# Performance work log

Measured on AMD Instinct MI355X. Metric: run time of the kernel, lower is better.

The kernel has to match this reference:

```python
import jax, jax.numpy as jnp
import numpy as np

D_MODEL, EMB_DIM, MLP_ORDER, SEQ_LEN, BATCH = 768, 3, 16, 8192, 8


def setup_inputs() -> dict:
    key = jax.random.key(0)
    ks = jax.random.split(key, 12)
    L = SEQ_LEN
    # PositionalEmbedding buffers (deterministic, as in __init__)
    t = jnp.linspace(0.0, 1.0, L)[None, :, None]                      # [1, L, 1]
    bands = (EMB_DIM - 1) // 2                                        # = 1
    t_long = jnp.linspace(0.0, L - 1.0, L)[None, :, None]
    w = 2.0 * jnp.pi * t_long / L
    f = jnp.linspace(1e-4, bands - 1.0, bands)[None, None]
    zc = jnp.exp(-1j * f * w)
    z = jnp.concatenate([t, zc.real, zc.imag], axis=-1).astype(jnp.float32)  # [1, L, 3]
    # ExponentialModulation deltas (deterministic)
    max_decay = jnp.log(0.01) / 0.3
    min_decay = jnp.log(0.01) / 1.5
    deltas = jnp.linspace(min_decay, max_decay, D_MODEL)[None, None].astype(jnp.float32)  # [1,1,D]
    s = 0.1
    return {
        "x": jax.random.normal(ks[0], (BATCH, D_MODEL, L), jnp.float32),
        "L": L,
        "z": z,
        "t": t.astype(jnp.float32),
        "deltas": deltas,
        "freq": jnp.ones((1, MLP_ORDER), jnp.float32),
        "W0": jax.random.normal(ks[1], (EMB_DIM, MLP_ORDER), jnp.float32) * s,
        "b0": jax.random.normal(ks[2], (MLP_ORDER,), jnp.float32) * s,
        "W1": jax.random.normal(ks[3], (MLP_ORDER, MLP_ORDER), jnp.float32) * s,
        "b1": jax.random.normal(ks[4], (MLP_ORDER,), jnp.float32) * s,
        "W2": jax.random.normal(ks[5], (MLP_ORDER, MLP_ORDER), jnp.float32) * s,
        "b2": jax.random.normal(ks[6], (MLP_ORDER,), jnp.float32) * s,
        "W3": jax.random.normal(ks[7], (MLP_ORDER, D_MODEL), jnp.float32) * s,
        "b3": jax.random.normal(ks[8], (D_MODEL,), jnp.float32) * s,
        "bias": jax.random.normal(ks[9], (D_MODEL,), jnp.float32),
    }


def reference(x, L, z, t, deltas, freq, W0, b0, W1, b1, W2, b2, W3, b3, bias):
    # filter generation: MLP with shared Sin activation, then exponential modulation
    zl = z[:, :L]
    h = jnp.sin(freq * (zl @ W0 + b0))
    h = jnp.sin(freq * (h @ W1 + b1))
    h = jnp.sin(freq * (h @ W2 + b2))
    h = h @ W3 + b3                               # [1, L, D]
    h = h * jnp.exp(-t[:, :L] * jnp.abs(deltas))  # exponential modulation
    k = h[0].T                                    # [D, L]
    # fftconv: causal long convolution via zero-padded FFT + skip x*bias
    fft_size = 2 * L
    y = jnp.fft.irfft(jnp.fft.rfft(x, n=fft_size) * jnp.fft.rfft(k, n=fft_size), n=fft_size)[..., :L]
    return y + x * bias[:, None]
```

## Files before the change

### kernel.cpp

```cpp
#include <hip/hip_runtime.h>
#include <math.h>


#define LSEQ 8192
#define NCH 768
#define NBATCH 8
#define NT 512

#define OFF_TWB  0
#define OFF_TW16 1024
#define OFF_TL   5124
#define OFF_TWC  6660
#define OFF_H    10240
#define OFF_KF   141312

typedef float cplx __attribute__((ext_vector_type(2)));

__device__ __forceinline__ cplx cmul(cplx a, cplx b){
    return cplx{a.x, a.x} * b + cplx{a.y, a.y} * cplx{-b.y, b.x};
}
__device__ __forceinline__ cplx mni(cplx a){ return cplx{a.y, -a.x}; }

__device__ __forceinline__ void wave_sync(){
    asm volatile("s_waitcnt lgkmcnt(0)" ::: "memory");
}
__device__ __forceinline__ void fence(){
    asm volatile("" ::: "memory");
}

__device__ __forceinline__ int IDX14(int i){ return i ^ (((i>>4) ^ (i>>8)) & 14); }
__device__ __forceinline__ int drev(int k){
    return ((k & 15) << 9) | (((k >> 4) & 15) << 5) | (((k >> 8) & 15) << 1) | (k >> 12);
}

#define C1 0.923879532511286756f
#define S1 0.382683432365089772f
#define R2 0.707106781186547524f

template<bool FULL>
__device__ __forceinline__ void dft16(cplx q[16]) {
    if constexpr (FULL) {
#pragma unroll
        for (int j = 0; j < 8; ++j) { cplx u=q[j], v=q[j+8]; q[j]=u+v; q[j+8]=u-v; }
    }
    q[9]  = cmul(q[9],  cplx{ C1,-S1});
    q[10] = cmul(q[10], cplx{ R2,-R2});
    q[11] = cmul(q[11], cplx{ S1,-C1});
    q[12] = mni(q[12]);
    q[13] = cmul(q[13], cplx{-S1,-C1});
    q[14] = cmul(q[14], cplx{-R2,-R2});
    q[15] = cmul(q[15], cplx{-C1,-S1});
#pragma unroll
    for (int b = 0; b < 16; b += 8) {
#pragma unroll
        for (int j = 0; j < 4; ++j) { cplx u=q[b+j], v=q[b+j+4]; q[b+j]=u+v; q[b+j+4]=u-v; }
        q[b+5] = cmul(q[b+5], cplx{ R2,-R2});
        q[b+6] = mni(q[b+6]);
        q[b+7] = cmul(q[b+7], cplx{-R2,-R2});
    }
#pragma unroll
    for (int b = 0; b < 16; b += 4) {
        cplx u0=q[b], v0=q[b+2], u1=q[b+1], v1=q[b+3];
        q[b]=u0+v0; q[b+2]=u0-v0;
        q[b+1]=u1+v1; q[b+3]=mni(u1-v1);
    }
#pragma unroll
    for (int b = 0; b < 16; b += 2) { cplx u=q[b], v=q[b+1]; q[b]=u+v; q[b+1]=u-v; }
}

template<int PASS>
__device__ __forceinline__ int psb(int t) {
    if constexpr (PASS == 0) {
        return t ^ (((t>>4) ^ (t>>8)) & 14);
    } else if constexpr (PASS == 1) {
        int p = t & 31, hb = t >> 5;
        return ((hb<<9) | p) ^ (((p>>4) ^ (hb<<1)) & 14);
    } else {
        int h = t >> 1;
        return ((h<<5) | (t&1)) ^ (((h<<1) ^ (h>>3)) & 14);
    }
}
template<int PASS>
__device__ __forceinline__ int paddr(int sb, int r) {
    if constexpr (PASS == 0)      return (sb ^ (2*(r&7))) + (r<<9);
    else if constexpr (PASS == 1) return (sb ^ (2*(r&7))) + (r<<5);
    else                          return sb ^ (r<<1);
}

template<int PASS, bool DIT, bool PRUNED>
__device__ __forceinline__ void r16p(cplx* lds, const cplx (*twT)[68],
                                     const cplx (&twA)[15], int t) {
    static constexpr int RV[16] = {0,8,4,12,2,10,6,14,1,9,5,13,3,11,7,15};
    const int sb = psb<PASS>(t);
    int rL = 0;
    if constexpr (PASS == 1) { rL = t & 31; }
    else if constexpr (PASS == 2) { rL = 64 + (t & 1); }
    cplx q[16];
    if constexpr (PRUNED) {
#pragma unroll
        for (int r = 0; r < 8; ++r) { q[r] = lds[paddr<PASS>(sb, r)]; q[r+8] = q[r]; }
    } else {
#pragma unroll
        for (int r = 0; r < 16; ++r) q[r] = lds[paddr<PASS>(sb, r)];
    }
    if constexpr (DIT) {
#pragma unroll
        for (int m = 1; m < 16; ++m) {
            cplx w = (PASS == 0) ? twA[m-1] : twT[m][rL];
            q[m] = cmul(q[m], w);
        }
        dft16<true>(q);
    } else {
        dft16<!PRUNED>(q);
#pragma unroll
        for (int m = 1; m < 16; ++m) {
            cplx w = (PASS == 0) ? twA[m-1] : twT[m][rL];
            q[RV[m]] = cmul(q[RV[m]], w);
        }
    }
#pragma unroll
    for (int m = 0; m < 16; ++m) lds[paddr<PASS>(sb, m)] = q[RV[m]];
}

template<int PASS, bool DIT, bool PRUNED>
__device__ __forceinline__ void r16pp(cplx* l0, cplx* l1, const cplx (*twT)[68],
                                      const cplx (&twA)[15], int t) {
    r16p<PASS, DIT, PRUNED>(l0, twT, twA, t);
    fence();
    r16p<PASS, DIT, PRUNED>(l1, twT, twA, t);
}

__device__ __forceinline__ void load_twT(cplx (*twT)[68], const float* __restrict__ ws, int tid) {
    const cplx* gTWB = (const cplx*)(ws + OFF_TWB);
    const cplx* gTL  = (const cplx*)(ws + OFF_TL);
    const cplx* gTWC = (const cplx*)(ws + OFF_TWC);
    for (int idx = tid; idx < 16*66; idx += NT) {
        int r = idx >> 4, m = idx & 15;
        cplx v;
        if (r < 32)      v = gTWB[(r << 4) + m];
        else if (r < 64) v = gTL[((r - 32) << 4) + m];
        else             v = gTWC[((r - 64) << 4) + m];
        twT[m][r] = v;
    }
}

__device__ __forceinline__ void make_twA(cplx (&twA)[15], const cplx (*twT)[68], int t) {
    const int rL = 32 + (t & 31);
    const int rH = (t >> 5) << 1;
#pragma unroll
    for (int m = 1; m < 16; ++m) twA[m-1] = cmul(twT[m][rL], twT[m][rH]);
}

__device__ __forceinline__ void specpair(cplx V1, cplx V2, float4 kv, cplx W,
                                         cplx& o1, cplx& o2) {
    cplx Eh = V1 + cplx{V2.x, -V2.y};
    cplx Oh = cplx{V1.y + V2.y, V2.x - V1.x};
    cplx S = cplx{kv.x, kv.y};
    float a = W.x*kv.z, b = W.y*kv.w, cc = W.x*kv.w, dd = W.y*kv.z;
    cplx T  = cplx{a - b, cc + dd};
    cplx T2 = cplx{a + b, cc - dd};
    cplx Ep = cmul(Eh, S) + cmul(Oh, T);
    cplx Op = cmul(Eh, T2) + cmul(Oh, S);
    o1 = cplx{Ep.y + Op.x, Ep.x - Op.y};
    o2 = cplx{Op.x - Ep.y, Ep.x + Op.y};
}

__device__ __forceinline__ void spec_rows(float4* l4, int sA, int sB,
                                          float4 kvk, float4 kvj, cplx W, cplx Wj) {
    float4 fA = l4[sA], fB = l4[sB];
    cplx uA = {fA.x, fA.y}, vA = {fA.z, fA.w};
    cplx uB = {fB.x, fB.y}, vB = {fB.z, fB.w};
    cplx Vk = uA + vA, Vk4 = uA - vA;
    cplx Vj = uB + vB, Vj4 = uB - vB;
    cplx r1, r2, r1j, r2j;
    specpair(Vk, Vj4, kvk, W,  r1,  r2);
    specpair(Vj, Vk4, kvj, Wj, r1j, r2j);
    cplx a0 = r1 + r2j, a1 = r1 - r2j;
    cplx b0 = r1j + r2, b1 = r1j - r2;
    l4[sA] = make_float4(a0.x, a0.y, a1.x, a1.y);
    l4[sB] = make_float4(b0.x, b0.y, b1.x, b1.y);
}

__device__ __forceinline__ void spec_dc(float4* l4, float4 kv) {
    float4 f = l4[0];
    cplx u = {f.x, f.y}, v = {f.z, f.w};
    cplx V0 = u + v, VN = u - v;
    float U0 = V0.x + V0.y, UL = V0.x - V0.y;
    float re = U0*kv.x + UL*kv.y;
    float im = U0*kv.x - UL*kv.y;
    cplx s0 = {im, re};
    cplx P = {VN.x*kv.z + VN.y*kv.w, VN.x*kv.w - VN.y*kv.z};
    cplx s1 = {-P.y, P.x};
    cplx a = s0 + s1, b = s0 - s1;
    l4[0] = make_float4(a.x, a.y, b.x, b.y);
}

__device__ __forceinline__ void filt_store(const float4* l4, float4* kf, int k, int jj,
                                           int sA, int sB, cplx W, cplx Wj,
                                           float sc, float eb) {
    float4 fA = l4[sA], fB = l4[sB];
    cplx uA = {fA.x, fA.y}, vA = {fA.z, fA.w};
    cplx uB = {fB.x, fB.y}, vB = {fB.z, fB.w};
    cplx Vk = uA + vA, Vk4 = uA - vA;
    cplx Vj = uB + vB, Vj4 = uB - vB;
    {
        cplx E = {Vk.x + Vj4.x + eb, Vk.y - Vj4.y};
        cplx O = {Vk.y + Vj4.y, Vj4.x - Vk.x};
        cplx D = cmul(W, O);
        kf[k] = make_float4(E.x*sc, E.y*sc, D.x*sc, D.y*sc);
    }
    {
        cplx E = {Vj.x + Vk4.x + eb, Vj.y - Vk4.y};
        cplx O = {Vj.y + Vk4.y, Vk4.x - Vj.x};
        cplx D = cmul(Wj, O);
        kf[jj] = make_float4(E.x*sc, E.y*sc, D.x*sc, D.y*sc);
    }
}
__device__ __forceinline__ void filt_dc(const float4* l4, float4* kf, float bc) {
    float4 f = l4[0];
    cplx u = {f.x, f.y}, v = {f.z, f.w};
    cplx V0 = u + v, VN = u - v;
    kf[0] = make_float4((V0.x + V0.y + bc)/16384.f, (V0.x - V0.y + bc)/16384.f,
                        (VN.x + bc)/8192.f, -VN.y/8192.f);
}

__global__ __launch_bounds__(512) void k_pre(const float* __restrict__ z, const float* __restrict__ freq,
        const float* __restrict__ W0, const float* __restrict__ b0,
        const float* __restrict__ W1, const float* __restrict__ b1,
        const float* __restrict__ W2, const float* __restrict__ b2,
        float* __restrict__ ws, float* __restrict__ H) {
    __shared__ double2 lA[128], lB[128];
    const int t = threadIdx.x;
    if (blockIdx.x == 0) {
        const double K = -2.0 * 3.14159265358979323846 / 16384.0;
        if (t < 128)      { double a = K * (double)(t << 7); lA[t] = make_double2(cos(a), sin(a)); }
        else if (t < 256) { int b = t - 128; double a = K * (double)b; lB[b] = make_double2(cos(a), sin(a)); }
        __syncthreads();
        auto wf = [&](int e) -> float2 {
            e &= 16383;
            double2 A = lA[e >> 7], B = lB[e & 127];
            return make_float2((float)(A.x*B.x - A.y*B.y), (float)(A.x*B.y + A.y*B.x));
        };
        float2* tw16 = (float2*)(ws + OFF_TW16);
        for (int k = t; k <= 2048; k += 512) tw16[k] = wf(k);
        if (t < 32) {
            float2* rowL = (float2*)(ws + OFF_TL)  + (t << 4);
            float2* rowB = (float2*)(ws + OFF_TWB) + (t << 4);
#pragma unroll
            for (int m = 0; m < 16; ++m) { rowL[m] = wf(2*t*m); rowB[m] = wf(32*t*m); }
        } else if (t < 34) {
            int c2 = t - 32;
            float2* rowC = (float2*)(ws + OFF_TWC) + (c2 << 4);
#pragma unroll
            for (int m = 0; m < 16; ++m) rowC[m] = wf(512*c2*m);
        }
    } else {
        const int j = ((blockIdx.x - 1) << 9) + t;
        const float z0 = z[j*3+0], z1 = z[j*3+1], z2 = z[j*3+2];
        float h[16], g[16];
#pragma unroll
        for (int m = 0; m < 16; ++m)
            h[m] = sinf(freq[m] * (z0*W0[m] + z1*W0[16+m] + z2*W0[32+m] + b0[m]));
#pragma unroll
        for (int m = 0; m < 16; ++m) {
            float a = b1[m];
#pragma unroll
            for (int p = 0; p < 16; ++p) a += h[p] * W1[p*16+m];
            g[m] = sinf(freq[m] * a);
        }
#pragma unroll
        for (int m = 0; m < 16; ++m) {
            float a = b2[m];
#pragma unroll
            for (int p = 0; p < 16; ++p) a += g[p] * W2[p*16+m];
            h[m] = sinf(freq[m] * a);
        }
        float4* hp = (float4*)(H + (j << 4));
        hp[0] = make_float4(h[0],  h[1],  h[2],  h[3]);
        hp[1] = make_float4(h[4],  h[5],  h[6],  h[7]);
        hp[2] = make_float4(h[8],  h[9],  h[10], h[11]);
        hp[3] = make_float4(h[12], h[13], h[14], h[15]);
    }
}

__global__ __launch_bounds__(NT) void k_filter(const float* __restrict__ H, const float* __restrict__ t,
        const float* __restrict__ deltas, const float* __restrict__ W3,
        const float* __restrict__ b3, const float* __restrict__ bias,
        const float* __restrict__ ws, float* __restrict__ KfF) {
    __shared__ alignas(16) cplx lds2[2][LSEQ];
    __shared__ cplx twT[16][68];
    const int c0 = blockIdx.x << 1, c1 = c0 + 1;
    const int tid = threadIdx.x;
    cplx* l0 = lds2[0];
    cplx* l1 = lds2[1];
    float4* l04 = (float4*)l0;
    float4* l14 = (float4*)l1;
    load_twT(twT, ws, tid);
    float w30[16], w31[16];
#pragma unroll
    for (int m = 0; m < 16; ++m) { w30[m] = W3[m*NCH + c0]; w31[m] = W3[m*NCH + c1]; }
    const float b30 = b3[c0], b31 = b3[c1];
    const float ad0 = fabsf(deltas[c0]), ad1 = fabsf(deltas[c1]);
    const float bc0 = bias[c0], bc1 = bias[c1];
    const int sbA = psb<0>(tid);
#pragma unroll 1
    for (int j = 0; j < 8; ++j) {
        int n = tid + (j << 9);
        const float4* hp = (const float4*)(H + (n << 5));
        float sA0 = b30, sB0 = b30, sA1 = b31, sB1 = b31;
#pragma unroll
        for (int q = 0; q < 4; ++q) {
            float4 a = hp[q];
            float4 b = hp[4+q];
            sA0 += a.x*w30[4*q] + a.y*w30[4*q+1] + a.z*w30[4*q+2] + a.w*w30[4*q+3];
            sB0 += b.x*w30[4*q] + b.y*w30[4*q+1] + b.z*w30[4*q+2] + b.w*w30[4*q+3];
            sA1 += a.x*w31[4*q] + a.y*w31[4*q+1] + a.z*w31[4*q+2] + a.w*w31[4*q+3];
            sB1 += b.x*w31[4*q] + b.y*w31[4*q+1] + b.z*w31[4*q+2] + b.w*w31[4*q+3];
        }
        float2 tv = ((const float2*)t)[n];
        int a0 = paddr<0>(sbA, j);
        float e0 = expf(-tv.x*ad0), e1 = expf(-tv.y*ad0);
        float e2 = expf(-tv.x*ad1), e3 = expf(-tv.y*ad1);
        l0[a0] = cplx{sA0 * e0, sB0 * e1};
        l1[a0] = cplx{sA1 * e2, sB1 * e3};
    }
    __syncthreads();
    cplx twA[15];
    make_twA(twA, twT, tid);
    r16pp<0,false,true >(l0, l1, twT, twA, tid); __syncthreads();
    r16pp<1,false,false>(l0, l1, twT, twA, tid); wave_sync();
    r16pp<2,false,false>(l0, l1, twT, twA, tid); __syncthreads();

    float4* kf0 = (float4*)KfF + (size_t)c0 * 4096;
    float4* kf1 = (float4*)KfF + (size_t)c1 * 4096;
    const cplx* tw16 = (const cplx*)(ws + OFF_TW16);
    const float sc = 1.0f / 32768.0f;
#pragma unroll 1
    for (int it = 0; it < 4; ++it) {
        int k  = tid + 1 + (it << 9);
        int jj = 4096 - k;
        int sA = IDX14(drev(k)) >> 1, sB = IDX14(drev(jj)) >> 1;
        cplx W  = tw16[k];
        cplx Wj = cplx{-W.y, -W.x};
        filt_store(l04, kf0, k, jj, sA, sB, W, Wj, sc, 2.0f*bc0);
        filt_store(l14, kf1, k, jj, sA, sB, W, Wj, sc, 2.0f*bc1);
    }
    if (tid == 0) { filt_dc(l04, kf0, bc0); filt_dc(l14, kf1, bc1); }
}

__global__ __launch_bounds__(NT) void k_main(const float* __restrict__ x, const float* __restrict__ ws,
        const float* __restrict__ KfF, float* __restrict__ out) {
    __shared__ alignas(16) cplx lds2[2][LSEQ];
    __shared__ cplx twT[16][68];
    const int bid = blockIdx.x;
    const int c = bid >> 1, half = bid & 1;
    const int tt = threadIdx.x;
    cplx* l0 = lds2[0];
    cplx* l1 = lds2[1];
    float4* l04 = (float4*)l0;
    float4* l14 = (float4*)l1;
    const float4* kf4 = (const float4*)KfF + (size_t)c * 4096;
    const cplx* tw16 = (const cplx*)(ws + OFF_TW16);
    const size_t rowstride = (size_t)NCH * LSEQ;
    const float* xbase = x + (size_t)(half*4) * rowstride + (size_t)c * LSEQ;
    float* obase = out + (size_t)(half*4) * rowstride + (size_t)c * LSEQ;

    const int EB = (tt << 1) ^ (((tt>>3) ^ (tt>>7)) & 14);

    load_twT(twT, ws, tt);
    __syncthreads();
    cplx twA[15];
    make_twA(twA, twT, tt);

#pragma unroll 1
    for (int pp = 0; pp < 2; ++pp) {
        const float4* xr0 = (const float4*)(xbase + (size_t)(2*pp)     * rowstride);
        const float4* xr1 = (const float4*)(xbase + (size_t)(2*pp + 1) * rowstride);
#pragma unroll
        for (int j = 0; j < 4; ++j) {
            int si = ((EB ^ (j<<2)) + (j<<10)) >> 1;
            l04[si] = xr0[tt + (j<<9)];
            l14[si] = xr1[tt + (j<<9)];
        }
        __syncthreads();
        r16pp<0,false,true >(l0, l1, twT, twA, tt); __syncthreads();
        r16pp<1,false,false>(l0, l1, twT, twA, tt); wave_sync();
        r16pp<2,false,false>(l0, l1, twT, twA, tt); __syncthreads();

#pragma unroll 1
        for (int it = 0; it < 4; ++it) {
            int k  = tt + 1 + (it << 9);
            int jj = 4096 - k;
            int sA = IDX14(drev(k)) >> 1, sB = IDX14(drev(jj)) >> 1;
            float4 kvk = kf4[k], kvj = kf4[jj];
            cplx W  = tw16[k];
            cplx Wj = cplx{-W.y, -W.x};
            spec_rows(l04, sA, sB, kvk, kvj, W, Wj);
            spec_rows(l14, sA, sB, kvk, kvj, W, Wj);
        }
        if (tt == 0) {
            float4 kv = kf4[0];
            spec_dc(l04, kv);
            spec_dc(l14, kv);
        }
        __syncthreads();

        r16pp<2,true,false>(l0, l1, twT, twA, tt); wave_sync();
        r16pp<1,true,false>(l0, l1, twT, twA, tt); __syncthreads();
        r16pp<0,true,false>(l0, l1, twT, twA, tt); __syncthreads();

        float4* o0 = (float4*)(obase + (size_t)(2*pp)     * rowstride);
        float4* o1 = (float4*)(obase + (size_t)(2*pp + 1) * rowstride);
#pragma unroll
        for (int j = 0; j < 4; ++j) {
            int si = ((EB ^ (j<<2)) + (j<<10)) >> 1;
            float4 f0 = l04[si], f1 = l14[si];
            o0[tt + (j<<9)] = make_float4(f0.y, f0.x, f0.w, f0.z);
            o1[tt + (j<<9)] = make_float4(f1.y, f1.x, f1.w, f1.z);
        }
        if (pp == 0) __syncthreads();
    }
}

extern "C" void kernel_launch(void* const* d_in, const int* in_sizes, int n_in,
                              void* d_out, int out_size, void* d_ws, size_t ws_size,
                              hipStream_t stream) {
    const float* x      = (const float*)d_in[0];
    const float* z      = (const float*)d_in[2];
    const float* t      = (const float*)d_in[3];
    const float* deltas = (const float*)d_in[4];
    const float* freq   = (const float*)d_in[5];
    const float* W0     = (const float*)d_in[6];
    const float* b0     = (const float*)d_in[7];
    const float* W1     = (const float*)d_in[8];
    const float* b1     = (const float*)d_in[9];
    const float* W2     = (const float*)d_in[10];
    const float* b2     = (const float*)d_in[11];
    const float* W3     = (const float*)d_in[12];
    const float* b3     = (const float*)d_in[13];
    const float* bias   = (const float*)d_in[14];
    float* out = (float*)d_out;
    float* ws  = (float*)d_ws;
    float* H   = ws + OFF_H;
    float* Kf  = ws + OFF_KF;

    hipLaunchKernelGGL(k_pre, dim3(17), dim3(512), 0, stream, z, freq, W0, b0, W1, b1, W2, b2, ws, H);
    hipLaunchKernelGGL(k_filter, dim3(NCH/2), dim3(NT), 0, stream, H, t, deltas, W3, b3, bias, ws, Kf);
    hipLaunchKernelGGL(k_main, dim3(NBATCH * NCH / 4), dim3(NT), 0, stream, x, ws, Kf, out);
}
```

Measured before the change: 595.6 us.

## Fuse filter spectrum generation into main convolution kernel, one channel per block

Removes the separate k_filter launch. Each k_main block now owns one channel: it builds that channel's modulated MLP filter, runs its forward FFT with the single-sequence r16p path and writes the spectrum to the workspace. It then loops over all 8 batch rows in 4 pairs, reusing the spectrum, instead of 2 blocks per channel doing 2 pairs each. This saves a kernel launch and the inter-kernel dependency. In exchange the grid shrinks to 768 blocks with longer per-block work, and the filter FFT runs unpaired at lower lane efficiency.

After: 574.9 us, median of 2. 1.04x faster.

```diff
diff --git a/kernel.cpp b/kernel.cpp
--- a/kernel.cpp
+++ b/kernel.cpp
@@ -283,99 +283,84 @@
     }
 }
 
-__global__ __launch_bounds__(NT) void k_filter(const float* __restrict__ H, const float* __restrict__ t,
-        const float* __restrict__ deltas, const float* __restrict__ W3,
-        const float* __restrict__ b3, const float* __restrict__ bias,
-        const float* __restrict__ ws, float* __restrict__ KfF) {
+__global__ __launch_bounds__(NT) void k_main(const float* __restrict__ x, const float* __restrict__ H,
+        const float* __restrict__ t, const float* __restrict__ deltas,
+        const float* __restrict__ W3, const float* __restrict__ b3,
+        const float* __restrict__ bias, const float* __restrict__ ws,
+        float* __restrict__ KfF, float* __restrict__ out) {
     __shared__ alignas(16) cplx lds2[2][LSEQ];
     __shared__ cplx twT[16][68];
-    const int c0 = blockIdx.x << 1, c1 = c0 + 1;
-    const int tid = threadIdx.x;
-    cplx* l0 = lds2[0];
-    cplx* l1 = lds2[1];
-    float4* l04 = (float4*)l0;
-    float4* l14 = (float4*)l1;
-    load_twT(twT, ws, tid);
-    float w30[16], w31[16];
-#pragma unroll
-    for (int m = 0; m < 16; ++m) { w30[m] = W3[m*NCH + c0]; w31[m] = W3[m*NCH + c1]; }
-    const float b30 = b3[c0], b31 = b3[c1];
-    const float ad0 = fabsf(deltas[c0]), ad1 = fabsf(deltas[c1]);
-    const float bc0 = bias[c0], bc1 = bias[c1];
-    const int sbA = psb<0>(tid);
-#pragma unroll 1
-    for (int j = 0; j < 8; ++j) {
-        int n = tid + (j << 9);
-        const float4* hp = (const float4*)(H + (n << 5));
-        float sA0 = b30, sB0 = b30, sA1 = b31, sB1 = b31;
-#pragma unroll
-        for (int q = 0; q < 4; ++q) {
-            float4 a = hp[q];
-            float4 b = hp[4+q];
-            sA0 += a.x*w30[4*q] + a.y*w30[4*q+1] + a.z*w30[4*q+2] + a.w*w30[4*q+3];
-            sB0 += b.x*w30[4*q] + b.y*w30[4*q+1] + b.z*w30[4*q+2] + b.w*w30[4*q+3];
-            sA1 += a.x*w31[4*q] + a.y*w31[4*q+1] + a.z*w31[4*q+2] + a.w*w31[4*q+3];
-            sB1 += b.x*w31[4*q] + b.y*w31[4*q+1] + b.z*w31[4*q+2] + b.w*w31[4*q+3];
-        }
-        float2 tv = ((const float2*)t)[n];
-        int a0 = paddr<0>(sbA, j);
-        float e0 = expf(-tv.x*ad0), e1 = expf(-tv.y*ad0);
-        float e2 = expf(-tv.x*ad1), e3 = expf(-tv.y*ad1);
-        l0[a0] = cplx{sA0 * e0, sB0 * e1};
-        l1[a0] = cplx{sA1 * e2, sB1 * e3};
-    }
-    __syncthreads();
-    cplx twA[15];
-    make_twA(twA, twT, tid);
-    r16pp<0,false,true >(l0, l1, twT, twA, tid); __syncthreads();
-    r16pp<1,false,false>(l0, l1, twT, twA, tid); wave_sync();
-    r16pp<2,false,false>(l0, l1, twT, twA, tid); __syncthreads();
-
-    float4* kf0 = (float4*)KfF + (size_t)c0 * 4096;
-    float4* kf1 = (float4*)KfF + (size_t)c1 * 4096;
-    const cplx* tw16 = (const cplx*)(ws + OFF_TW16);
-    const float sc = 1.0f / 32768.0f;
-#pragma unroll 1
-    for (int it = 0; it < 4; ++it) {
-        int k  = tid + 1 + (it << 9);
-        int jj = 4096 - k;
-        int sA = IDX14(drev(k)) >> 1, sB = IDX14(drev(jj)) >> 1;
-        cplx W  = tw16[k];
-        cplx Wj = cplx{-W.y, -W.x};
-        filt_store(l04, kf0, k, jj, sA, sB, W, Wj, sc, 2.0f*bc0);
-        filt_store(l14, kf1, k, jj, sA, sB, W, Wj, sc, 2.0f*bc1);
-    }
-    if (tid == 0) { filt_dc(l04, kf0, bc0); filt_dc(l14, kf1, bc1); }
-}
-
-__global__ __launch_bounds__(NT) void k_main(const float* __restrict__ x, const float* __restrict__ ws,
-        const float* __restrict__ KfF, float* __restrict__ out) {
-    __shared__ alignas(16) cplx lds2[2][LSEQ];
-    __shared__ cplx twT[16][68];
-    const int bid = blockIdx.x;
-    const int c = bid >> 1, half = bid & 1;
+    const int c = blockIdx.x;
     const int tt = threadIdx.x;
     cplx* l0 = lds2[0];
     cplx* l1 = lds2[1];
     float4* l04 = (float4*)l0;
     float4* l14 = (float4*)l1;
-    const float4* kf4 = (const float4*)KfF + (size_t)c * 4096;
+    float4* kf4 = (float4*)KfF + (size_t)c * 4096;
     const cplx* tw16 = (const cplx*)(ws + OFF_TW16);
     const size_t rowstride = (size_t)NCH * LSEQ;
-    const float* xbase = x + (size_t)(half*4) * rowstride + (size_t)c * LSEQ;
-    float* obase = out + (size_t)(half*4) * rowstride + (size_t)c * LSEQ;
+    const float* xcol = x + (size_t)c * LSEQ;
+    float* ocol = out + (size_t)c * LSEQ;
+    const float sc = 1.0f / 32768.0f;
 
     const int EB = (tt << 1) ^ (((tt>>3) ^ (tt>>7)) & 14);
+    const int sbA = psb<0>(tt);
 
     load_twT(twT, ws, tt);
+
+    {
+        float4 w3a = make_float4(W3[0*NCH+c],  W3[1*NCH+c],  W3[2*NCH+c],  W3[3*NCH+c]);
+        float4 w3b = make_float4(W3[4*NCH+c],  W3[5*NCH+c],  W3[6*NCH+c],  W3[7*NCH+c]);
+        float4 w3c = make_float4(W3[8*NCH+c],  W3[9*NCH+c],  W3[10*NCH+c], W3[11*NCH+c]);
+        float4 w3d = make_float4(W3[12*NCH+c], W3[13*NCH+c], W3[14*NCH+c], W3[15*NCH+c]);
+        const float b3c = b3[c];
+        const float ad = fabsf(deltas[c]);
+#pragma unroll 1
+        for (int j = 0; j < 8; ++j) {
+            int n = tt + (j << 9);
+            const float4* hp = (const float4*)(H + (n << 5));
+            float4 p0 = hp[0], p1 = hp[1], p2 = hp[2], p3 = hp[3];
+            float4 q0 = hp[4], q1 = hp[5], q2 = hp[6], q3 = hp[7];
+            float s0 = b3c + p0.x*w3a.x + p0.y*w3a.y + p0.z*w3a.z + p0.w*w3a.w
+                           + p1.x*w3b.x + p1.y*w3b.y + p1.z*w3b.z + p1.w*w3b.w
+                           + p2.x*w3c.x + p2.y*w3c.y + p2.z*w3c.z + p2.w*w3c.w
+                           + p3.x*w3d.x + p3.y*w3d.y + p3.z*w3d.z + p3.w*w3d.w;
+            float s1 = b3c + q0.x*w3a.x + q0.y*w3a.y + q0.z*w3a.z + q0.w*w3a.w
+                           + q1.x*w3b.x + q1.y*w3b.y + q1.z*w3b.z + q1.w*w3b.w
+                           + q2.x*w3c.x + q2.y*w3c.y + q2.z*w3c.z + q2.w*w3c.w
+                           + q3.x*w3d.x + q3.y*w3d.y + q3.z*w3d.z + q3.w*w3d.w;
+            float2 tv = ((const float2*)t)[n];
+            l0[paddr<0>(sbA, j)] = cplx{s0 * expf(-tv.x*ad), s1 * expf(-tv.y*ad)};
+        }
+    }
     __syncthreads();
     cplx twA[15];
     make_twA(twA, twT, tt);
 
+    r16p<0,false,true >(l0, twT, twA, tt); __syncthreads();
+    r16p<1,false,false>(l0, twT, twA, tt); wave_sync();
+    r16p<2,false,false>(l0, twT, twA, tt); __syncthreads();
+
+    {
+        const float bc = bias[c];
+        const float eb = 2.0f * bc;
 #pragma unroll 1
-    for (int pp = 0; pp < 2; ++pp) {
-        const float4* xr0 = (const float4*)(xbase + (size_t)(2*pp)     * rowstride);
-        const float4* xr1 = (const float4*)(xbase + (size_t)(2*pp + 1) * rowstride);
+        for (int it = 0; it < 4; ++it) {
+            int k  = tt + 1 + (it << 9);
+            int jj = 4096 - k;
+            int sA = IDX14(drev(k)) >> 1, sB = IDX14(drev(jj)) >> 1;
+            cplx W  = tw16[k];
+            cplx Wj = cplx{-W.y, -W.x};
+            filt_store(l04, kf4, k, jj, sA, sB, W, Wj, sc, eb);
+        }
+        if (tt == 0) filt_dc(l04, kf4, bc);
+    }
+    __syncthreads();
+
+#pragma unroll 1
+    for (int pp = 0; pp < 4; ++pp) {
+        const float4* xr0 = (const float4*)(xcol + (size_t)(2*pp)     * rowstride);
+        const float4* xr1 = (const float4*)(xcol + (size_t)(2*pp + 1) * rowstride);
 #pragma unroll
         for (int j = 0; j < 4; ++j) {
             int si = ((EB ^ (j<<2)) + (j<<10)) >> 1;
@@ -409,8 +394,8 @@
         r16pp<1,true,false>(l0, l1, twT, twA, tt); __syncthreads();
         r16pp<0,true,false>(l0, l1, twT, twA, tt); __syncthreads();
 
-        float4* o0 = (float4*)(obase + (size_t)(2*pp)     * rowstride);
-        float4* o1 = (float4*)(obase + (size_t)(2*pp + 1) * rowstride);
+        float4* o0 = (float4*)(ocol + (size_t)(2*pp)     * rowstride);
+        float4* o1 = (float4*)(ocol + (size_t)(2*pp + 1) * rowstride);
 #pragma unroll
         for (int j = 0; j < 4; ++j) {
             int si = ((EB ^ (j<<2)) + (j<<10)) >> 1;
@@ -418,7 +403,7 @@
             o0[tt + (j<<9)] = make_float4(f0.y, f0.x, f0.w, f0.z);
             o1[tt + (j<<9)] = make_float4(f1.y, f1.x, f1.w, f1.z);
         }
-        if (pp == 0) __syncthreads();
+        if (pp < 3) __syncthreads();
     }
 }
 
@@ -445,6 +430,5 @@
     float* Kf  = ws + OFF_KF;
 
     hipLaunchKernelGGL(k_pre, dim3(17), dim3(512), 0, stream, z, freq, W0, b0, W1, b1, W2, b2, ws, H);
-    hipLaunchKernelGGL(k_filter, dim3(NCH/2), dim3(NT), 0, stream, H, t, deltas, W3, b3, bias, ws, Kf);
-    hipLaunchKernelGGL(k_main, dim3(NBATCH * NCH / 4), dim3(NT), 0, stream, x, ws, Kf, out);
-}
+    hipLaunchKernelGGL(k_main, dim3(NCH), dim3(NT), 0, stream, x, H, t, deltas, W3, b3, bias, ws, Kf, out);
+}
```
